# Performance work log

Hardware: AMD Instinct MI355X
Metric: run time of the kernel (lower is better)

Reference implementation:

```python
import jax, jax.numpy as jnp
import numpy as np

N_NODES = 10000
N_EDGES = 50000
N_GRAPHS = 64
NODE_DIM = 32
EDGE_DIM = 16
HID = 64
EDGE_HID = 128
OUT_DIM = 1
T_STEPS = 3       # message-passing rounds
S2S_STEPS = 6     # Set2Set processing steps


def setup_inputs() -> dict:
    key = jax.random.key(0)
    ks = jax.random.split(key, 24)
    def w(k, shape, scale):
        return (jax.random.normal(k, shape, dtype=jnp.float32) * scale)
    inp = {}
    inp["node_features"] = jax.random.normal(ks[0], (N_NODES, NODE_DIM), dtype=jnp.float32)
    inp["edge_features"] = jax.random.normal(ks[1], (N_EDGES, EDGE_DIM), dtype=jnp.float32)
    inp["edge_index"] = jax.random.randint(ks[2], (2, N_EDGES), 0, N_NODES, dtype=jnp.int32)
    # sorted, fully-covering graph assignment (nodes of each graph are contiguous)
    inp["batch_indices"] = ((jnp.arange(N_NODES) * N_GRAPHS) // N_NODES).astype(jnp.int32)
    # input projection
    inp["W_proj"] = w(ks[3], (NODE_DIM, HID), 1.0 / np.sqrt(NODE_DIM))
    inp["b_proj"] = jnp.zeros((HID,), jnp.float32)
    # edge network MLP: edge_dim -> edge_hid -> hid*hid
    inp["W_e1"] = w(ks[4], (EDGE_DIM, EDGE_HID), 1.0 / np.sqrt(EDGE_DIM))
    inp["b_e1"] = jnp.zeros((EDGE_HID,), jnp.float32)
    inp["W_e2"] = w(ks[5], (EDGE_HID, HID * HID), 0.01)
    inp["b_e2"] = jnp.zeros((HID * HID,), jnp.float32)
    # GRU cell (torch layout: 3*hid rows = r,z,n)
    inp["W_gih"] = w(ks[6], (3 * HID, HID), 1.0 / np.sqrt(HID))
    inp["W_ghh"] = w(ks[7], (3 * HID, HID), 1.0 / np.sqrt(HID))
    inp["b_gih"] = jnp.zeros((3 * HID,), jnp.float32)
    inp["b_ghh"] = jnp.zeros((3 * HID,), jnp.float32)
    # LSTM cell (torch layout: 4*hid rows = i,f,g,o), input 2*hid
    inp["W_lih"] = w(ks[8], (4 * HID, 2 * HID), 1.0 / np.sqrt(HID))
    inp["W_lhh"] = w(ks[9], (4 * HID, HID), 1.0 / np.sqrt(HID))
    inp["b_lih"] = jnp.zeros((4 * HID,), jnp.float32)
    inp["b_lhh"] = jnp.zeros((4 * HID,), jnp.float32)
    # readout MLP: 2*hid -> hid -> out
    inp["W_m1"] = w(ks[10], (2 * HID, HID), 1.0 / np.sqrt(2 * HID))
    inp["b_m1"] = jnp.zeros((HID,), jnp.float32)
    inp["W_m2"] = w(ks[11], (HID, OUT_DIM), 1.0 / np.sqrt(HID))
    inp["b_m2"] = jnp.zeros((OUT_DIM,), jnp.float32)
    return inp


def _scatter_softmax(e, idx, n_seg):
    mx = jax.ops.segment_max(e, idx, num_segments=n_seg)
    ex = jnp.exp(e - mx[idx])
    s = jax.ops.segment_sum(ex, idx, num_segments=n_seg)
    return ex / (s[idx] + 1e-16)


def _mpnn_forward(node_features, edge_features, edge_index, batch_indices,
                  W_proj, b_proj, W_e1, b_e1, W_e2, b_e2,
                  W_gih, W_ghh, b_gih, b_ghh,
                  W_lih, W_lhh, b_lih, b_lhh,
                  W_m1, b_m1, W_m2, b_m2):
    n_nodes = node_features.shape[0]
    dst = edge_index[0]  # receiving node v
    src = edge_index[1]  # sending node w

    # input projection
    h = node_features @ W_proj + b_proj                       # (N, H)

    # edge network: per-edge transformation matrix A(e_vw) (depends only on edge feats)
    A = jax.nn.relu(edge_features @ W_e1 + b_e1) @ W_e2 + b_e2
    A = A.reshape(-1, HID, HID)                               # (E, H, H)

    # T rounds: gather senders, per-edge bmm, scatter-add to receivers, GRU update
    for _ in range(T_STEPS):
        msgs = jnp.einsum('eij,ej->ei', A, h[src])            # (E, H)
        m = jax.ops.segment_sum(msgs, dst, num_segments=n_nodes)
        gx = m @ W_gih.T + b_gih                              # (N, 3H)
        gh = h @ W_ghh.T + b_ghh
        xr, xz, xn = jnp.split(gx, 3, axis=-1)
        hr, hz, hn = jnp.split(gh, 3, axis=-1)
        r = jax.nn.sigmoid(xr + hr)
        z = jax.nn.sigmoid(xz + hz)
        n = jnp.tanh(xn + r * hn)
        h = (1.0 - z) * n + z * h

    # Set2Set readout
    hs = jnp.zeros((N_GRAPHS, HID), h.dtype)
    cs = jnp.zeros((N_GRAPHS, HID), h.dtype)
    rs = jnp.zeros((N_GRAPHS, HID), h.dtype)
    for _ in range(S2S_STEPS):
        q = hs[batch_indices]                                 # (N, H)
        e = jnp.sum(h * q, axis=-1)                           # (N,)
        a = _scatter_softmax(e, batch_indices, N_GRAPHS)
        rs = jax.ops.segment_sum(a[:, None] * h, batch_indices, num_segments=N_GRAPHS)
        x = jnp.concatenate([hs, rs], axis=-1)                # (G, 2H)
        gates = x @ W_lih.T + b_lih + hs @ W_lhh.T + b_lhh    # (G, 4H)
        i, f, g, o = jnp.split(gates, 4, axis=-1)
        cs = jax.nn.sigmoid(f) * cs + jax.nn.sigmoid(i) * jnp.tanh(g)
        hs = jax.nn.sigmoid(o) * jnp.tanh(cs)
    ge = jnp.concatenate([hs, rs], axis=-1)                   # (G, 2H)
    return jax.nn.relu(ge @ W_m1 + b_m1) @ W_m2 + b_m2        # (G, out)


def reference(node_features, edge_features, edge_index, batch_indices,
              W_proj, b_proj, W_e1, b_e1, W_e2, b_e2,
              W_gih, W_ghh, b_gih, b_ghh,
              W_lih, W_lhh, b_lih, b_lhh,
              W_m1, b_m1, W_m2, b_m2):
    return _mpnn_forward(node_features, edge_features, edge_index, batch_indices,
                         W_proj, b_proj, W_e1, b_e1, W_e2, b_e2,
                         W_gih, W_ghh, b_gih, b_ghh,
                         W_lih, W_lhh, b_lih, b_lhh,
                         W_m1, b_m1, W_m2, b_m2)
```

## Files before the change

kernel.cpp:

```cpp
#include <hip/hip_runtime.h>

#define N_NODES   10000
#define N_EDGES   50000
#define N_GRAPHS  64
#define NODE_DIM  32
#define EDGE_DIM  16
#define HID       64
#define EHID      128
#define T_STEPS   3
#define S2S_STEPS 6

typedef _Float16 half_t;
typedef _Float16 f16x8 __attribute__((ext_vector_type(8)));
typedef float    f32x4 __attribute__((ext_vector_type(4)));

__device__ __forceinline__ float sigf(float x){ return 1.0f/(1.0f + expf(-x)); }

__global__ void k_zero(float* p, int n){
  int i = blockIdx.x*256 + threadIdx.x;
  if (i < n) p[i] = 0.0f;
}

__global__ void k_proj(const float* __restrict__ nf, const float* __restrict__ Wp,
                       const float* __restrict__ bp, float* __restrict__ h){
  int idx = blockIdx.x*256 + threadIdx.x;
  if (idx >= N_NODES*HID) return;
  int n = idx >> 6;
  int c = idx & 63;
  float acc = bp[c];
  const float* row = nf + (size_t)n*NODE_DIM;
  for (int j = 0; j < NODE_DIM; ++j)
    acc = fmaf(row[j], Wp[j*HID + c], acc);
  h[idx] = acc;
}

__global__ void k_tw2(const float* __restrict__ W2, float* __restrict__ Mm){
  int idx = blockIdx.x*256 + threadIdx.x;
  if (idx >= 64*8192) return;
  int j = idx >> 13; int o = idx & 8191; int k = o >> 6; int i = o & 63;
  Mm[idx] = W2[(size_t)k*4096 + i*64 + j];
}

__global__ void k_w2bt(const float* __restrict__ W2, half_t* __restrict__ BT){
  int idx = blockIdx.x*256 + threadIdx.x;
  if (idx >= 512*2*64*8) return;
  int j    = idx & 7;
  int lane = (idx >> 3) & 63;
  int tk   = (idx >> 9) & 1;
  int tn   = idx >> 10;
  int k = tk*32 + ((lane >> 4) << 3) + j;
  int o = tn*16 + (lane & 15);
  BT[idx] = (half_t)W2[(size_t)(o >> 6)*4096 + (o & 63)*64 + k];
}

__global__ void k_h2a(const float* __restrict__ h, half_t* __restrict__ AT){
  int idx = blockIdx.x*256 + threadIdx.x;
  if (idx >= 625*2*64*8) return;
  int j    = idx & 7;
  int lane = (idx >> 3) & 63;
  int tk   = (idx >> 9) & 1;
  int tm   = idx >> 10;
  int mrow = tm*16 + (lane & 15);
  int k    = tk*32 + ((lane >> 4) << 3) + j;
  AT[idx] = (half_t)h[(size_t)mrow*64 + k];
}

__global__ void k_twg(const float* __restrict__ Wg, const float* __restrict__ Wh,
                      float* __restrict__ WgT, float* __restrict__ WhT){
  int idx = blockIdx.x*256 + threadIdx.x;
  if (idx >= 192*64) return;
  int row = idx >> 6;
  int j   = idx & 63;
  WgT[j*192 + row] = Wg[(size_t)row*64 + j];
  WhT[j*192 + row] = Wh[(size_t)row*64 + j];
}

__global__ void k_ehid(const float* __restrict__ ef, const float* __restrict__ W1,
                       const float* __restrict__ b1, float* __restrict__ Hid){
  int idx = blockIdx.x*256 + threadIdx.x;
  if (idx >= N_EDGES*EHID) return;
  int e = idx >> 7, c = idx & 127;
  float acc = b1[c];
  const float* er = ef + (size_t)e*EDGE_DIM;
  for (int j = 0; j < EDGE_DIM; ++j)
    acc = fmaf(er[j], W1[j*EHID + c], acc);
  Hid[idx] = fmaxf(acc, 0.0f);
}

__global__ void k_ehid16(const float* __restrict__ ef, const float* __restrict__ W1,
                         const float* __restrict__ b1, half_t* __restrict__ Hid16){
  int idx = blockIdx.x*256 + threadIdx.x;
  if (idx >= N_EDGES*EHID) return;
  int e = idx >> 7, c = idx & 127;
  float acc = b1[c];
  const float* er = ef + (size_t)e*EDGE_DIM;
  for (int j = 0; j < EDGE_DIM; ++j)
    acc = fmaf(er[j], W1[j*EHID + c], acc);
  Hid16[idx] = (half_t)fmaxf(acc, 0.0f);
}

__global__ void k_bh(const float* __restrict__ h, const float* __restrict__ be2,
                     float* __restrict__ bh){
  int idx = blockIdx.x*256 + threadIdx.x;
  if (idx >= N_NODES*HID) return;
  int n = idx >> 6, i = idx & 63;
  float acc = 0.0f;
  const float* row = be2 + (size_t)i*64;
  const float* hr  = h + (size_t)n*64;
  for (int j = 0; j < 64; ++j)
    acc = fmaf(row[j], hr[j], acc);
  bh[idx] = acc;
}

__global__ void k_hist(const int* __restrict__ ei, int* __restrict__ deg){
  int e = blockIdx.x*256 + threadIdx.x;
  if (e >= N_EDGES) return;
  atomicAdd(&deg[ei[N_EDGES + e]], 1);
}

__global__ void k_scan(const int* __restrict__ deg, int* __restrict__ rowptr,
                       int* __restrict__ cursor){
  __shared__ int part[256];
  int t = threadIdx.x;
  int base = t*40;
  int s = 0;
  for (int i = 0; i < 40; ++i){
    int idx = base + i;
    if (idx < N_NODES) s += deg[idx];
  }
  part[t] = s;
  __syncthreads();
  for (int off = 1; off < 256; off <<= 1){
    int v = (t >= off) ? part[t - off] : 0;
    __syncthreads();
    part[t] += v;
    __syncthreads();
  }
  int run = (t > 0) ? part[t - 1] : 0;
  for (int i = 0; i < 40; ++i){
    int idx = base + i;
    if (idx < N_NODES){
      rowptr[idx] = run;
      cursor[idx] = run;
      run += deg[idx];
    }
  }
  if (t == 255) rowptr[N_NODES] = run;
}

__global__ void k_scatter(const int* __restrict__ ei, int* __restrict__ cursor,
                          int* __restrict__ csr){
  int e = blockIdx.x*256 + threadIdx.x;
  if (e >= N_EDGES) return;
  int src = ei[N_EDGES + e];
  int pos = atomicAdd(&cursor[src], 1);
  csr[pos] = e;
}

__global__ void MPNN_55705725829535_kernel(const half_t* __restrict__ AT,
                                           const half_t* __restrict__ BT,
                                           const int* __restrict__ rowptr,
                                           const int* __restrict__ csr,
                                           const int* __restrict__ ei,
                                           const half_t* __restrict__ Hid16,
                                           const float* __restrict__ bh,
                                           float* __restrict__ m){
  __shared__ half_t Ct[16][4][520];
  __shared__ int dstW[4][16];
  int wv   = threadIdx.x >> 6;
  int lane = threadIdx.x & 63;
  int quad = lane >> 4;
  int colb = lane & 15;
  int tm = blockIdx.x;
  int q  = blockIdx.y;

  const f16x8* Ab = (const f16x8*)AT + (size_t)tm*128;
  f16x8 a0 = Ab[lane];
  f16x8 a1 = Ab[64 + lane];
  #pragma unroll
  for (int kt = 0; kt < 4; ++kt){
    f32x4 acc[8];
    #pragma unroll
    for (int jj = 0; jj < 8; ++jj){
      acc[jj][0]=0.f; acc[jj][1]=0.f; acc[jj][2]=0.f; acc[jj][3]=0.f;
    }
    #pragma unroll
    for (int jj = 0; jj < 8; ++jj){
      int ke = kt*32 + wv*8 + jj;
      int tn = ke*4 + q;
      const f16x8* Bb = (const f16x8*)BT + (size_t)tn*128;
      acc[jj] = __builtin_amdgcn_mfma_f32_16x16x32_f16(a0, Bb[lane],      acc[jj], 0, 0, 0);
      acc[jj] = __builtin_amdgcn_mfma_f32_16x16x32_f16(a1, Bb[64 + lane], acc[jj], 0, 0, 0);
    }
    #pragma unroll
    for (int r = 0; r < 4; ++r){
      int node = quad*4 + r;
      f16x8 v;
      #pragma unroll
      for (int jj = 0; jj < 8; ++jj) v[jj] = (half_t)acc[jj][r];
      *(f16x8*)&Ct[node][kt][(wv*16 + colb)*8] = v;
    }
  }
  __syncthreads();

  for (int c = 0; c < 4; ++c){
    int node = wv*4 + c;
    int s = tm*16 + node;
    int beg  = rowptr[s];
    int endp = rowptr[s + 1];
    if (beg == endp) continue;
    f16x8 B[4];
    #pragma unroll
    for (int kt = 0; kt < 4; ++kt)
      B[kt] = *(const f16x8*)&Ct[node][kt][lane*8];
    float bhc = bh[(size_t)s*64 + q*16 + colb];
    for (int gbeg = beg; gbeg < endp; gbeg += 16){
      int gn = endp - gbeg; if (gn > 16) gn = 16;
      if (lane < 16)
        dstW[wv][lane] = (lane < gn) ? ei[csr[gbeg + lane]] : -1;
      f16x8 A[4];
      if (colb < gn){
        int e = csr[gbeg + colb];
        const f16x8* Hb = (const f16x8*)(Hid16 + (size_t)e*128) + quad;
        #pragma unroll
        for (int kt = 0; kt < 4; ++kt)
          A[kt] = Hb[kt*4];
      } else {
        #pragma unroll
        for (int kt = 0; kt < 4; ++kt)
          #pragma unroll
          for (int p = 0; p < 8; ++p) A[kt][p] = (half_t)0;
      }
      f32x4 acc;
      acc[0]=0.f; acc[1]=0.f; acc[2]=0.f; acc[3]=0.f;
      #pragma unroll
      for (int kt = 0; kt < 4; ++kt)
        acc = __builtin_amdgcn_mfma_f32_16x16x32_f16(A[kt], B[kt], acc, 0, 0, 0);
      #pragma unroll
      for (int r = 0; r < 4; ++r){
        int jrow = quad*4 + r;
        if (jrow < gn){
          int d = dstW[wv][jrow];
          atomicAdd(&m[(size_t)d*64 + q*16 + colb], acc[r] + bhc);
        }
      }
    }
  }
}

__global__ void k_cgemm(const float* __restrict__ h, const float* __restrict__ Mm,
                        half_t* __restrict__ C, int lo, int hi){
  __shared__ float hs[16][64];
  int n0 = lo + blockIdx.x*16;
  int o0 = blockIdx.y*256 + threadIdx.x;
  for (int idx = threadIdx.x; idx < 16*64; idx += 256){
    int nn = idx >> 6, j = idx & 63;
    int node = n0 + nn;
    hs[nn][j] = (node < hi) ? h[(size_t)node*64 + j] : 0.0f;
  }
  __syncthreads();
  float acc0[16], acc1[16];
  #pragma unroll
  for (int nn = 0; nn < 16; ++nn){ acc0[nn] = 0.0f; acc1[nn] = 0.0f; }
  for (int j4 = 0; j4 < 16; ++j4){
    const float* M0 = Mm + (size_t)(j4*4)*8192;
    float a0 = M0[o0],            b0 = M0[o0 + 4096];
    float a1 = M0[8192 + o0],     b1 = M0[8192 + o0 + 4096];
    float a2 = M0[2*8192 + o0],   b2 = M0[2*8192 + o0 + 4096];
    float a3 = M0[3*8192 + o0],   b3 = M0[3*8192 + o0 + 4096];
    #pragma unroll
    for (int nn = 0; nn < 16; ++nn){
      float4 hv = *(const float4*)&hs[nn][j4*4];
      acc0[nn] = fmaf(hv.x, a0, acc0[nn]);
      acc1[nn] = fmaf(hv.x, b0, acc1[nn]);
      acc0[nn] = fmaf(hv.y, a1, acc0[nn]);
      acc1[nn] = fmaf(hv.y, b1, acc1[nn]);
      acc0[nn] = fmaf(hv.z, a2, acc0[nn]);
      acc1[nn] = fmaf(hv.z, b2, acc1[nn]);
      acc0[nn] = fmaf(hv.w, a3, acc0[nn]);
      acc1[nn] = fmaf(hv.w, b3, acc1[nn]);
    }
  }
  #pragma unroll
  for (int nn = 0; nn < 16; ++nn){
    int node = n0 + nn;
    if (node < hi){
      half_t* Cr = C + (size_t)(node - lo)*8192;
      Cr[o0]        = (half_t)acc0[nn];
      Cr[o0 + 4096] = (half_t)acc1[nn];
    }
  }
}

__global__ void k_msg_csr(const int* __restrict__ rowptr,
                          const int* __restrict__ csr,
                          const int* __restrict__ ei,
                          const float* __restrict__ Hid,
                          const half_t* __restrict__ C,
                          const float* __restrict__ bh,
                          float* __restrict__ m, int lo, int hi){
  __shared__ float hidL[4][8][128];
  int wave = threadIdx.x >> 6;
  int lane = threadIdx.x & 63;
  int s = lo + blockIdx.x*4 + wave;
  if (s >= hi) return;
  int beg = rowptr[s];
  int endp = rowptr[s + 1];
  if (beg == endp) return;
  float bhv = bh[(size_t)s*64 + lane];
  const half_t* Cb = C + (size_t)(s - lo)*8192 + lane;
  float (*hl)[128] = hidL[wave];
  for (int gbeg = beg; gbeg < endp; gbeg += 8){
    int gn = endp - gbeg; if (gn > 8) gn = 8;
    int dsts[8];
    int e0 = csr[gbeg];
    #pragma unroll
    for (int j = 0; j < 8; ++j){
      int e = (j < gn) ? csr[gbeg + j] : e0;
      dsts[j] = ei[e];
      hl[j][lane]      = Hid[(size_t)e*128 + lane];
      hl[j][lane + 64] = Hid[(size_t)e*128 + 64 + lane];
    }
    float acc[8];
    #pragma unroll
    for (int j = 0; j < 8; ++j) acc[j] = 0.0f;
    #pragma unroll 4
    for (int k = 0; k < 128; ++k){
      float c = (float)Cb[k*64];
      #pragma unroll
      for (int j = 0; j < 8; ++j)
        acc[j] = fmaf(hl[j][k], c, acc[j]);
    }
    for (int j = 0; j < gn; ++j)
      atomicAdd(&m[(size_t)dsts[j]*64 + lane], acc[j] + bhv);
  }
}

__global__ void k_msg_fb(const int* __restrict__ ei, const float* __restrict__ ef,
                         const float* __restrict__ W1, const float* __restrict__ b1,
                         const float* __restrict__ W2, const float* __restrict__ be2,
                         const float* __restrict__ h, float* __restrict__ m){
  __shared__ float HidL[EHID];
  __shared__ __align__(16) float hsL[HID];
  int e = blockIdx.x;
  int t = threadIdx.x;
  int src = ei[N_EDGES + e];
  int dst = ei[e];
  {
    float a0 = b1[t];
    float a1 = b1[t + 64];
    const float* er = ef + (size_t)e*EDGE_DIM;
    for (int j = 0; j < EDGE_DIM; ++j){
      float ev = er[j];
      a0 = fmaf(ev, W1[j*EHID + t],      a0);
      a1 = fmaf(ev, W1[j*EHID + t + 64], a1);
    }
    HidL[t]      = fmaxf(a0, 0.0f);
    HidL[t + 64] = fmaxf(a1, 0.0f);
    hsL[t] = h[(size_t)src*64 + t];
  }
  __syncthreads();
  float acc = 0.0f;
  for (int k = 0; k < EHID; ++k){
    float s = HidL[k];
    if (s != 0.0f){
      const float* w = W2 + (size_t)k*4096 + t*64;
      float partial = 0.0f;
      for (int j = 0; j < 64; ++j)
        partial = fmaf(hsL[j], w[j], partial);
      acc = fmaf(s, partial, acc);
    }
  }
  {
    const float* w = be2 + (size_t)t*64;
    for (int j = 0; j < 64; ++j)
      acc = fmaf(hsL[j], w[j], acc);
  }
  atomicAdd(&m[(size_t)dst*64 + t], acc);
}

__global__ void k_gru(float* __restrict__ h, const float* __restrict__ m,
                      const float* __restrict__ WgT, const float* __restrict__ WhT,
                      const float* __restrict__ bg, const float* __restrict__ bhb){
  __shared__ float mld[16][64];
  __shared__ float hld[16][64];
  int t  = threadIdx.x;
  int i  = t & 63;
  int wv = t >> 6;
  int n0 = blockIdx.x*16;
  for (int idx = t; idx < 16*64; idx += 256){
    int nn = idx >> 6, j = idx & 63;
    int node = n0 + nn;
    mld[nn][j] = m[(size_t)node*64 + j];
    hld[nn][j] = h[(size_t)node*64 + j];
  }
  __syncthreads();
  float xr[4], xz[4], xn[4], hr[4], hz[4], hn[4];
  #pragma unroll
  for (int c = 0; c < 4; ++c){
    xr[c] = bg[i];  xz[c] = bg[64 + i];  xn[c] = bg[128 + i];
    hr[c] = bhb[i]; hz[c] = bhb[64 + i]; hn[c] = bhb[128 + i];
  }
  for (int j = 0; j < 64; ++j){
    const float* wg = WgT + j*192;
    const float* wh = WhT + j*192;
    float wgr = wg[i], wgz = wg[64 + i], wgn = wg[128 + i];
    float whr = wh[i], whz = wh[64 + i], whn = wh[128 + i];
    #pragma unroll
    for (int c = 0; c < 4; ++c){
      int nn = wv*4 + c;
      float mj = mld[nn][j];
      float hj = hld[nn][j];
      xr[c] = fmaf(mj, wgr, xr[c]);
      xz[c] = fmaf(mj, wgz, xz[c]);
      xn[c] = fmaf(mj, wgn, xn[c]);
      hr[c] = fmaf(hj, whr, hr[c]);
      hz[c] = fmaf(hj, whz, hz[c]);
      hn[c] = fmaf(hj, whn, hn[c]);
    }
  }
  #pragma unroll
  for (int c = 0; c < 4; ++c){
    int nn = wv*4 + c;
    float r  = sigf(xr[c] + hr[c]);
    float z  = sigf(xz[c] + hz[c]);
    float nv = tanhf(xn[c] + r*hn[c]);
    h[(size_t)(n0 + nn)*64 + i] = (1.0f - z)*nv + z*hld[nn][i];
  }
}

__global__ void k_s2s(const float* __restrict__ h,
                      const float* __restrict__ Wli, const float* __restrict__ Wlh,
                      const float* __restrict__ bli, const float* __restrict__ blh,
                      const float* __restrict__ Wm1, const float* __restrict__ bm1,
                      const float* __restrict__ Wm2, const float* __restrict__ bm2,
                      float* __restrict__ out){
  __shared__ float hc[157*65];
  __shared__ float ea[160];
  __shared__ float x[192];
  __shared__ float gpart[512];
  __shared__ float rsp[8][64];
  __shared__ float wredA[8];
  __shared__ float wredB[8];
  __shared__ float hsb[64];
  __shared__ float csb[64];
  __shared__ float rsb[64];
  int g = blockIdx.x;
  int t = threadIdx.x;
  int lane = t & 63;
  int wv   = t >> 6;
  int start = (g*N_NODES + 63) >> 6;
  int end   = ((g + 1)*N_NODES + 63) >> 6;
  int cnt = end - start;
  const float* hg = h + (size_t)start*64;
  for (int idx = t; idx < cnt*64; idx += 512)
    hc[(idx >> 6)*65 + (idx & 63)] = hg[idx];
  if (t < 64){ hsb[t] = 0.0f; csb[t] = 0.0f; rsb[t] = 0.0f; }
  __syncthreads();
  for (int step = 0; step < S2S_STEPS; ++step){
    float ev = -1e30f;
    if (t < cnt){
      float a = 0.0f;
      const float* hr = &hc[t*65];
      for (int i = 0; i < 64; ++i) a = fmaf(hr[i], hsb[i], a);
      ev = a;
    }
    float v = ev;
    for (int o = 32; o > 0; o >>= 1) v = fmaxf(v, __shfl_xor(v, o));
    if (lane == 0) wredA[wv] = v;
    __syncthreads();
    float mx = wredA[0];
    #pragma unroll
    for (int i = 1; i < 8; ++i) mx = fmaxf(mx, wredA[i]);
    float ex = (t < cnt) ? expf(ev - mx) : 0.0f;
    float sv = ex;
    for (int o = 32; o > 0; o >>= 1) sv += __shfl_xor(sv, o);
    if (lane == 0) wredB[wv] = sv;
    __syncthreads();
    float ssum = 0.0f;
    #pragma unroll
    for (int i = 0; i < 8; ++i) ssum += wredB[i];
    if (t < cnt) ea[t] = ex / (ssum + 1e-16f);
    __syncthreads();
    {
      int n0 = wv*20;
      int n1 = n0 + 20; if (n1 > cnt) n1 = cnt;
      float r = 0.0f;
      for (int n = n0; n < n1; ++n)
        r = fmaf(ea[n], hc[n*65 + lane], r);
      rsp[wv][lane] = r;
    }
    __syncthreads();
    if (t < 64){
      float r = rsp[0][t] + rsp[1][t] + rsp[2][t] + rsp[3][t]
              + rsp[4][t] + rsp[5][t] + rsp[6][t] + rsp[7][t];
      rsb[t] = r;
      x[t]        = hsb[t];
      x[64 + t]   = r;
      x[128 + t]  = hsb[t];
    }
    __syncthreads();
    {
      int gate = t & 255;
      int half = t >> 8;
      float gl = 0.0f;
      if (half == 0){
        const float* wr = Wli + (size_t)gate*128;
        for (int jj = 0; jj < 96; ++jj) gl = fmaf(x[jj], wr[jj], gl);
      } else {
        const float* wr = Wli + (size_t)gate*128;
        for (int jj = 96; jj < 128; ++jj) gl = fmaf(x[jj], wr[jj], gl);
        const float* wh = Wlh + (size_t)gate*64;
        for (int jj = 0; jj < 64; ++jj) gl = fmaf(x[128 + jj], wh[jj], gl);
      }
      gpart[t] = gl;
    }
    __syncthreads();
    if (t < 64){
      float iv = sigf (gpart[t]       + gpart[t + 256]       + bli[t]       + blh[t]);
      float fv = sigf (gpart[64 + t]  + gpart[64 + t + 256]  + bli[64 + t]  + blh[64 + t]);
      float gv = tanhf(gpart[128 + t] + gpart[128 + t + 256] + bli[128 + t] + blh[128 + t]);
      float ov = sigf (gpart[192 + t] + gpart[192 + t + 256] + bli[192 + t] + blh[192 + t]);
      float c  = fv*csb[t] + iv*gv;
      csb[t] = c;
      hsb[t] = ov*tanhf(c);
    }
    __syncthreads();
  }
  float rv = 0.0f;
  if (t < 64){
    float v = bm1[t];
    for (int j = 0; j < 64; ++j) v = fmaf(hsb[j], Wm1[(size_t)j*64 + t],        v);
    for (int j = 0; j < 64; ++j) v = fmaf(rsb[j], Wm1[(size_t)(64 + j)*64 + t], v);
    v = fmaxf(v, 0.0f);
    rv = v * Wm2[t];
  }
  for (int o = 32; o > 0; o >>= 1) rv += __shfl_xor(rv, o);
  if (lane == 0) wredA[wv] = rv;
  __syncthreads();
  if (t == 0) out[g] = wredA[0] + wredA[1] + wredA[2] + wredA[3]
                     + wredA[4] + wredA[5] + wredA[6] + wredA[7] + bm2[0];
}

extern "C" void kernel_launch(void* const* d_in, const int* in_sizes, int n_in,
                              void* d_out, int out_size, void* d_ws, size_t ws_size,
                              hipStream_t stream){
  (void)in_sizes; (void)n_in; (void)out_size;

  const float* nf  = (const float*)d_in[0];
  const float* ef  = (const float*)d_in[1];
  const int*   ei  = (const int*)d_in[2];
  const float* Wp  = (const float*)d_in[4];
  const float* bp  = (const float*)d_in[5];
  const float* We1 = (const float*)d_in[6];
  const float* be1 = (const float*)d_in[7];
  const float* We2 = (const float*)d_in[8];
  const float* be2 = (const float*)d_in[9];
  const float* Wg  = (const float*)d_in[10];
  const float* Wh  = (const float*)d_in[11];
  const float* bg  = (const float*)d_in[12];
  const float* bhb = (const float*)d_in[13];
  const float* Wli = (const float*)d_in[14];
  const float* Wlh = (const float*)d_in[15];
  const float* bli = (const float*)d_in[16];
  const float* blh = (const float*)d_in[17];
  const float* Wm1 = (const float*)d_in[18];
  const float* bm1 = (const float*)d_in[19];
  const float* Wm2 = (const float*)d_in[20];
  const float* bm2 = (const float*)d_in[21];

  float* out = (float*)d_out;
  float* ws  = (float*)d_ws;

  float* h    = ws;
  float* m    = ws + 640000;
  float* bh   = ws + 1280000;
  float* Mm   = ws + 1920000;
  float* WgT  = ws + 2444288;
  float* WhT  = ws + 2456576;
  float* Hid  = ws + 2468864;
  half_t* Hid16 = (half_t*)Hid;
  int*   deg    = (int*)(ws + 8868864);
  int*   rowptr = deg + 10000;
  int*   cursor = rowptr + 10001;
  int*   csr    = cursor + 10000;
  half_t* AT  = (half_t*)(ws + 8948880);
  half_t* BT  = (half_t*)(ws + 9268880);
  const size_t C_OFF = 9531024;
  half_t* C   = (half_t*)(ws + C_OFF);

  long long c_halves = ((long long)ws_size - (long long)C_OFF*4) / 2;
  int NC = (c_halves > 0) ? (int)(c_halves / 8192) : 0;
  if (NC > N_NODES) NC = N_NODES;
  int use_c_path = (NC >= 512);
  int use_mfma   = (NC >= N_NODES);

  k_proj<<<(N_NODES*HID + 255)/256, 256, 0, stream>>>(nf, Wp, bp, h);

  if (use_c_path){
    k_twg <<<(192*64 + 255)/256, 256, 0, stream>>>(Wg, Wh, WgT, WhT);
    k_zero<<<(10000 + 255)/256, 256, 0, stream>>>((float*)deg, 10000);
    k_hist<<<(N_EDGES + 255)/256, 256, 0, stream>>>(ei, deg);
    k_scan<<<1, 256, 0, stream>>>(deg, rowptr, cursor);
    k_scatter<<<(N_EDGES + 255)/256, 256, 0, stream>>>(ei, cursor, csr);
    if (use_mfma){
      k_ehid16<<<(N_EDGES*EHID + 255)/256, 256, 0, stream>>>(ef, We1, be1, Hid16);
      k_w2bt<<<(512*2*64*8 + 255)/256, 256, 0, stream>>>(We2, BT);
      for (int step = 0; step < T_STEPS; ++step){
        k_zero<<<(N_NODES*HID + 255)/256, 256, 0, stream>>>(m, N_NODES*HID);
        k_bh<<<(N_NODES*HID + 255)/256, 256, 0, stream>>>(h, be2, bh);
        k_h2a<<<(625*2*64*8 + 255)/256, 256, 0, stream>>>(h, AT);
        dim3 grid(625, 4);
        MPNN_55705725829535_kernel<<<grid, 256, 0, stream>>>(
            AT, BT, rowptr, csr, ei, Hid16, bh, m);
        k_gru<<<625, 256, 0, stream>>>(h, m, WgT, WhT, bg, bhb);
      }
    } else {
      k_ehid<<<(N_EDGES*EHID + 255)/256, 256, 0, stream>>>(ef, We1, be1, Hid);
      k_tw2<<<(64*8192)/256, 256, 0, stream>>>(We2, Mm);
      for (int step = 0; step < T_STEPS; ++step){
        k_zero<<<(N_NODES*HID + 255)/256, 256, 0, stream>>>(m, N_NODES*HID);
        k_bh<<<(N_NODES*HID + 255)/256, 256, 0, stream>>>(h, be2, bh);
        for (int lo = 0; lo < N_NODES; lo += NC){
          int hi = (lo + NC < N_NODES) ? lo + NC : N_NODES;
          int cnt = hi - lo;
          dim3 grid((cnt + 15)/16, 16);
          k_cgemm<<<grid, 256, 0, stream>>>(h, Mm, C, lo, hi);
          k_msg_csr<<<(cnt + 3)/4, 256, 0, stream>>>(
              rowptr, csr, ei, Hid, C, bh, m, lo, hi);
        }
        k_gru<<<625, 256, 0, stream>>>(h, m, WgT, WhT, bg, bhb);
      }
    }
  } else {
    k_twg <<<(192*64 + 255)/256, 256, 0, stream>>>(Wg, Wh, WgT, WhT);
    for (int step = 0; step < T_STEPS; ++step){
      k_zero<<<(N_NODES*HID + 255)/256, 256, 0, stream>>>(m, N_NODES*HID);
      k_msg_fb<<<N_EDGES, 64, 0, stream>>>(ei, ef, We1, be1, We2, be2, h, m);
      k_gru<<<625, 256, 0, stream>>>(h, m, WgT, WhT, bg, bhb);
    }
  }
  k_s2s<<<N_GRAPHS, 512, 0, stream>>>(h, Wli, Wlh, bli, blh,
                                      Wm1, bm1, Wm2, bm2, out);
}
```

Before: 601.2 us.

## Fuse per-step prep kernels and split message kernel tiles into half-node blocks

```diff
diff --git a/kernel.cpp b/kernel.cpp
--- a/kernel.cpp
+++ b/kernel.cpp
@@ -65,6 +65,28 @@
   AT[idx] = (half_t)h[(size_t)mrow*64 + k];
 }
 
+__global__ void k_prep(const float* __restrict__ h, const float* __restrict__ be2,
+                       float* __restrict__ m, float* __restrict__ bhp,
+                       half_t* __restrict__ AT){
+  int idx = blockIdx.x*256 + threadIdx.x;
+  if (idx >= N_NODES*HID) return;
+  m[idx] = 0.0f;
+  int n = idx >> 6, i = idx & 63;
+  float acc = 0.0f;
+  const float* row = be2 + (size_t)i*64;
+  const float* hr  = h + (size_t)n*64;
+  for (int j = 0; j < 64; ++j)
+    acc = fmaf(row[j], hr[j], acc);
+  bhp[idx] = acc;
+  int j    = idx & 7;
+  int lane = (idx >> 3) & 63;
+  int tk   = (idx >> 9) & 1;
+  int tm   = idx >> 10;
+  int mrow = tm*16 + (lane & 15);
+  int k    = tk*32 + ((lane >> 4) << 3) + j;
+  AT[idx] = (half_t)h[(size_t)mrow*64 + k];
+}
+
 __global__ void k_twg(const float* __restrict__ Wg, const float* __restrict__ Wh,
                       float* __restrict__ WgT, float* __restrict__ WhT){
   int idx = blockIdx.x*256 + threadIdx.x;
@@ -165,18 +187,21 @@
                                            const half_t* __restrict__ Hid16,
                                            const float* __restrict__ bh,
                                            float* __restrict__ m){
-  __shared__ half_t Ct[16][4][520];
+  __shared__ half_t Ct[8][4][520];
   __shared__ int dstW[4][16];
   int wv   = threadIdx.x >> 6;
   int lane = threadIdx.x & 63;
   int quad = lane >> 4;
   int colb = lane & 15;
-  int tm = blockIdx.x;
-  int q  = blockIdx.y;
-
-  const f16x8* Ab = (const f16x8*)AT + (size_t)tm*128;
-  f16x8 a0 = Ab[lane];
-  f16x8 a1 = Ab[64 + lane];
+  int tmb = blockIdx.x;
+  int q   = blockIdx.y;
+  int tile = tmb >> 1;
+  int hi   = tmb & 1;
+
+  int srcl = (lane & 48) | (hi << 3) | (lane & 7);
+  const f16x8* Ab = (const f16x8*)AT + (size_t)tile*128;
+  f16x8 a0 = Ab[srcl];
+  f16x8 a1 = Ab[64 + srcl];
   #pragma unroll
   for (int kt = 0; kt < 4; ++kt){
     f32x4 acc[8];
@@ -192,20 +217,22 @@
       acc[jj] = __builtin_amdgcn_mfma_f32_16x16x32_f16(a0, Bb[lane],      acc[jj], 0, 0, 0);
       acc[jj] = __builtin_amdgcn_mfma_f32_16x16x32_f16(a1, Bb[64 + lane], acc[jj], 0, 0, 0);
     }
-    #pragma unroll
-    for (int r = 0; r < 4; ++r){
-      int node = quad*4 + r;
-      f16x8 v;
+    if (quad < 2){
       #pragma unroll
-      for (int jj = 0; jj < 8; ++jj) v[jj] = (half_t)acc[jj][r];
-      *(f16x8*)&Ct[node][kt][(wv*16 + colb)*8] = v;
+      for (int r = 0; r < 4; ++r){
+        int node = quad*4 + r;
+        f16x8 v;
+        #pragma unroll
+        for (int jj = 0; jj < 8; ++jj) v[jj] = (half_t)acc[jj][r];
+        *(f16x8*)&Ct[node][kt][(wv*16 + colb)*8] = v;
+      }
     }
   }
   __syncthreads();
 
-  for (int c = 0; c < 4; ++c){
-    int node = wv*4 + c;
-    int s = tm*16 + node;
+  for (int c = 0; c < 2; ++c){
+    int node = wv*2 + c;
+    int s = tmb*8 + node;
     int beg  = rowptr[s];
     int endp = rowptr[s + 1];
     if (beg == endp) continue;
@@ -607,10 +634,8 @@
       k_ehid16<<<(N_EDGES*EHID + 255)/256, 256, 0, stream>>>(ef, We1, be1, Hid16);
       k_w2bt<<<(512*2*64*8 + 255)/256, 256, 0, stream>>>(We2, BT);
       for (int step = 0; step < T_STEPS; ++step){
-        k_zero<<<(N_NODES*HID + 255)/256, 256, 0, stream>>>(m, N_NODES*HID);
-        k_bh<<<(N_NODES*HID + 255)/256, 256, 0, stream>>>(h, be2, bh);
-        k_h2a<<<(625*2*64*8 + 255)/256, 256, 0, stream>>>(h, AT);
-        dim3 grid(625, 4);
+        k_prep<<<(N_NODES*HID + 255)/256, 256, 0, stream>>>(h, be2, m, bh, AT);
+        dim3 grid(1250, 4);
         MPNN_55705725829535_kernel<<<grid, 256, 0, stream>>>(
             AT, BT, rowptr, csr, ei, Hid16, bh, m);
         k_gru<<<625, 256, 0, stream>>>(h, m, WgT, WhT, bg, bhb);
```

Result: faster. 582.6 us (-3.1%).
